# Optimization experiments

Measured on AMD Instinct MI355X. Metric: run time of the kernel, lower is better.

## Reference

```python
import jax, jax.numpy as jnp
import numpy as np

C = 512
NUM_GROUPS = 32
EPS = 1e-6


def setup_inputs() -> dict:
    key = jax.random.key(0)
    ks = jax.random.split(key, 10)
    x = jax.random.normal(ks[0], (2, C, 64, 64), dtype=jnp.float32)
    s = 1.0 / np.sqrt(C)
    return {
        "x": x,
        "gn_gamma": jnp.ones((C,), jnp.float32),
        "gn_beta": jnp.zeros((C,), jnp.float32),
        "wq": jax.random.normal(ks[1], (C, C), jnp.float32) * s,
        "bq": jnp.zeros((C,), jnp.float32),
        "wk": jax.random.normal(ks[2], (C, C), jnp.float32) * s,
        "bk": jnp.zeros((C,), jnp.float32),
        "wv": jax.random.normal(ks[3], (C, C), jnp.float32) * s,
        "bv": jnp.zeros((C,), jnp.float32),
        "wo": jax.random.normal(ks[4], (C, C), jnp.float32) * s,
        "bo": jnp.zeros((C,), jnp.float32),
    }


def group_norm(x, gamma, beta):
    b, c, h, w = x.shape
    xg = x.reshape(b, NUM_GROUPS, c // NUM_GROUPS, h, w)
    mean = xg.mean(axis=(2, 3, 4), keepdims=True)
    var = xg.var(axis=(2, 3, 4), keepdims=True)
    xg = (xg - mean) * jax.lax.rsqrt(var + EPS)
    x = xg.reshape(b, c, h, w)
    return x * gamma[None, :, None, None] + beta[None, :, None, None]


def conv1x1(x, w, bias):
    # 1x1 conv == channel matmul: (b,c,h,w),(o,c) -> (b,o,h,w)
    return jnp.einsum('bchw,oc->bohw', x, w) + bias[None, :, None, None]


def reference(x, gn_gamma, gn_beta, wq, bq, wk, bk, wv, bv, wo, bo):
    b, c, h, w = x.shape
    hn = group_norm(x, gn_gamma, gn_beta)
    q = conv1x1(hn, wq, bq).reshape(b, c, h * w)  # (b,c,n)
    k = conv1x1(hn, wk, bk).reshape(b, c, h * w)
    v = conv1x1(hn, wv, bv).reshape(b, c, h * w)
    scale = int(c) ** (-0.5)
    # scores[b,i,j] = sum_c q[b,c,i] k[b,c,j]
    scores = jnp.einsum('bci,bcj->bij', q, k) * scale
    attn = jax.nn.softmax(scores, axis=2)
    out = jnp.einsum('bcj,bij->bci', v, attn).reshape(b, c, h, w)
    out = conv1x1(out, wo, bo)
    return x + out
```

## Files before the change

### kernel.cpp

```cpp
#include <hip/hip_runtime.h>

typedef unsigned short ushort_t;
typedef unsigned char uchar_t;
typedef __bf16 bf16x8 __attribute__((ext_vector_type(8)));
typedef float f32x4 __attribute__((ext_vector_type(4)));

__device__ __forceinline__ ushort_t f2bf(float f) {
  unsigned u = __float_as_uint(f);
  u += 0x7fff + ((u >> 16) & 1);
  return (ushort_t)(u >> 16);
}

__device__ __forceinline__ void gload16(const void* g, void* l) {
  __builtin_amdgcn_global_load_lds(
      (const __attribute__((address_space(1))) unsigned int*)g,
      (__attribute__((address_space(3))) unsigned int*)l, 16, 0, 0);
}

__global__ __launch_bounds__(256) void cvt_weights(
    const float* __restrict__ wq, const float* __restrict__ wk,
    const float* __restrict__ wv, const float* __restrict__ wo,
    const float* __restrict__ bq, const float* __restrict__ bk,
    ushort_t* __restrict__ dst, float* __restrict__ qkbias,
    float* __restrict__ stats2) {
  int b = blockIdx.x, t = threadIdx.x;
  if (b < 1024) {
    int i = b * 256 + t;
    dst[i]          = f2bf(wq[i]);
    dst[262144 + i] = f2bf(wk[i]);
    dst[524288 + i] = f2bf(wv[i]);
    dst[786432 + i] = f2bf(wo[i]);
  } else if (b < 1028) {
    int j = (b - 1024) * 256 + t;
    qkbias[j] = (j < 512) ? bq[j] : bk[j - 512];
  } else {
    if (t < 128) stats2[t] = 0.f;
  }
}

__global__ __launch_bounds__(256) void zero_f32(float* __restrict__ p) {
  p[blockIdx.x * 256 + threadIdx.x] = 0.f;
}

__global__ __launch_bounds__(256) void gn_stats_partial(const float* __restrict__ x,
                                                        float* __restrict__ stats2) {
  int bg = blockIdx.x >> 2, q = blockIdx.x & 3;
  const float4* p = (const float4*)(x + (size_t)bg * 65536 + q * 16384);
  float s = 0.f, ss = 0.f;
  for (int i = threadIdx.x; i < 4096; i += 256) {
    float4 v = p[i];
    s += v.x + v.y + v.z + v.w;
    ss += v.x * v.x + v.y * v.y + v.z * v.z + v.w * v.w;
  }
  for (int off = 32; off; off >>= 1) {
    s += __shfl_xor(s, off, 64);
    ss += __shfl_xor(ss, off, 64);
  }
  __shared__ float sh[8];
  int wave = threadIdx.x >> 6, lane = threadIdx.x & 63;
  if (lane == 0) { sh[wave] = s; sh[4 + wave] = ss; }
  __syncthreads();
  if (threadIdx.x == 0) {
    atomicAdd(&stats2[bg * 2], sh[0] + sh[1] + sh[2] + sh[3]);
    atomicAdd(&stats2[bg * 2 + 1], sh[4] + sh[5] + sh[6] + sh[7]);
  }
}

__global__ __launch_bounds__(64) void gn_finalize(const float* __restrict__ stats2,
                                                  float* __restrict__ stats) {
  int t = threadIdx.x;
  float s = stats2[t * 2], ss = stats2[t * 2 + 1];
  float mean = s * (1.f / 65536.f);
  float var = ss * (1.f / 65536.f) - mean * mean;
  stats[t * 2] = mean;
  stats[t * 2 + 1] = rsqrtf(var + 1e-6f);
}

__global__ __launch_bounds__(256) void gn_apply(
    const float* __restrict__ x, const float* __restrict__ gamma,
    const float* __restrict__ beta, const float* __restrict__ stats,
    ushort_t* __restrict__ hnT) {
  __shared__ float T[32][33];
  int i0 = blockIdx.x * 32, c0 = blockIdx.y * 32, b = blockIdx.z;
  int tx = threadIdx.x, ty = threadIdx.y;
#pragma unroll
  for (int k = 0; k < 4; k++) {
    int cl = ty + k * 8;
    int c = c0 + cl;
    int bg = (b * 32 + (c >> 4)) * 2;
    float mean = stats[bg], rstd = stats[bg + 1];
    float v = x[((size_t)(b * 512 + c)) * 4096 + i0 + tx];
    T[cl][tx] = (v - mean) * rstd * gamma[c] + beta[c];
  }
  __syncthreads();
#pragma unroll
  for (int k = 0; k < 4; k++) {
    int il = ty + k * 8;
    hnT[((size_t)b * 4096 + i0 + il) * 512 + c0 + tx] = f2bf(T[tx][il]);
  }
}

template <int BN>
__global__ __launch_bounds__(256) void gemm_abt(
    const ushort_t* __restrict__ A, long long sA, int lda,
    const ushort_t* __restrict__ B, long long sB, int ldb,
    int K, int N, int ldc,
    ushort_t* __restrict__ outB, long long sC,
    const float* __restrict__ bias, int bias_mode, float scale,
    float* __restrict__ outF, const float* __restrict__ resid,
    float* __restrict__ rowsum, const float* __restrict__ colscale,
    int swiz, int omode) {
  constexpr int CPW = (8 + BN / 16) / 4;
  constexpr int SB = (128 + BN) * 32;
  constexpr int MI = (BN == 128) ? 4 : 2;
  constexpr int NI = 4;
  __shared__ __align__(16) ushort_t Ls[2][SB];

  int bx = blockIdx.x, by = blockIdx.y, bz = blockIdx.z;
  if (swiz) {
    unsigned nx = gridDim.x, ny = gridDim.y;
    unsigned id = (blockIdx.z * ny + blockIdx.y) * nx + blockIdx.x;
    unsigned pb8 = (nx * ny) >> 3;
    unsigned c = id & 7, j = id >> 3;
    bz = j / pb8;
    unsigned jb = j - bz * pb8;
    unsigned jy = jb / nx;
    by = c * (ny >> 3) + jy;
    bx = jb - jy * nx;
  }

  int m0 = by * 128, n0 = bx * BN;
  int t = threadIdx.x;
  int lane = t & 63;
  int quad = lane >> 4, l16 = lane & 15;
  int wave = t >> 6;
  int wm = (BN == 128) ? (wave >> 1) * 64 : wave * 32;
  int wn = (BN == 128) ? (wave & 1) * 64 : 0;

  f32x4 acc[MI][NI];
#pragma unroll
  for (int i = 0; i < MI; i++)
#pragma unroll
    for (int j = 0; j < NI; j++)
#pragma unroll
      for (int r = 0; r < 4; r++) acc[i][j][r] = 0.f;

  const ushort_t* gp[CPW];
  int lofs[CPW];
  int crow = lane >> 2, skoff = (lane & 3) * 8;
#pragma unroll
  for (int i = 0; i < CPW; i++) {
    int c = wave * CPW + i;
    if (c < 8) {
      gp[i] = A + (size_t)bz * sA + (size_t)(m0 + c * 16 + crow) * lda + skoff;
      lofs[i] = c * 1024 + lane * 16;
    } else {
      int slot = (c - 8) * 16 + crow;
      int arow = (slot & ~63) + ((slot & 15) * 4) + ((slot & 63) >> 4);
      gp[i] = B + (size_t)bz * sB + (size_t)(n0 + arow) * ldb + skoff;
      lofs[i] = 8192 + (c - 8) * 1024 + lane * 16;
    }
  }
  char* lbase = (char*)&Ls[0][0];

#pragma unroll
  for (int i = 0; i < CPW; i++) gload16(gp[i], lbase + lofs[i]);

  for (int k0 = 0; k0 < K; k0 += 32) {
    int p = (k0 >> 5) & 1;
    __syncthreads();
    if (k0 + 32 < K) {
      int pofs = (p ^ 1) * (SB * 2);
#pragma unroll
      for (int i = 0; i < CPW; i++) gload16(gp[i] + k0 + 32, lbase + pofs + lofs[i]);
    }
    bf16x8 af[MI], bfr[NI];
#pragma unroll
    for (int i = 0; i < MI; i++)
      af[i] = *(const bf16x8*)&Ls[p][(wm + i * 16 + l16) * 32 + quad * 8];
#pragma unroll
    for (int j = 0; j < NI; j++)
      bfr[j] = *(const bf16x8*)&Ls[p][4096 + (wn + j * 16 + l16) * 32 + quad * 8];
#pragma unroll
    for (int mi = 0; mi < MI; mi++)
#pragma unroll
      for (int ni = 0; ni < NI; ni++)
        acc[mi][ni] = __builtin_amdgcn_mfma_f32_16x16x32_bf16(af[mi], bfr[ni], acc[mi][ni], 0, 0, 0);
  }

  size_t cbase = (size_t)bz * sC;
  int gnb = n0 + wn + l16 * 4;
  float cs4[4] = {1.f, 1.f, 1.f, 1.f};
  if (colscale) {
    float4 c4 = *(const float4*)&colscale[(size_t)bz * N + gnb];
    cs4[0] = 1.f / c4.x; cs4[1] = 1.f / c4.y; cs4[2] = 1.f / c4.z; cs4[3] = 1.f / c4.w;
  }
  float b4[4] = {0.f, 0.f, 0.f, 0.f};
  if (bias_mode == 2) {
    float4 t4 = *(const float4*)&bias[gnb];
    b4[0] = t4.x; b4[1] = t4.y; b4[2] = t4.z; b4[3] = t4.w;
  }
#pragma unroll
  for (int mi = 0; mi < MI; mi++) {
#pragma unroll
    for (int r = 0; r < 4; r++) {
      int m = m0 + wm + mi * 16 + quad * 4 + r;
      float rbias = (bias_mode == 1) ? bias[m] : 0.f;
      float v4[4];
      float rs = 0.f;
#pragma unroll
      for (int ni = 0; ni < NI; ni++) {
        float val = acc[mi][ni][r];
        if (colscale) val *= cs4[ni];
        val += (bias_mode == 2) ? b4[ni] : rbias;
        val *= scale;
        if (rowsum) { val = __expf(val) * 0.0625f; rs += val; }
        v4[ni] = val;
      }
      size_t idx = cbase + (size_t)m * ldc + gnb;
      if (omode == 1) {
        float4 rv = *(const float4*)&resid[idx];
        float4 ov = make_float4(v4[0] + rv.x, v4[1] + rv.y, v4[2] + rv.z, v4[3] + rv.w);
        *(float4*)&outF[idx] = ov;
      } else if (omode == 2) {
        unsigned w = __builtin_amdgcn_cvt_pk_fp8_f32(v4[0], v4[1], 0u, false);
        w = __builtin_amdgcn_cvt_pk_fp8_f32(v4[2], v4[3], w, true);
        *(unsigned*)&((uchar_t*)outB)[idx] = w;
      } else {
        unsigned lo = (unsigned)f2bf(v4[0]) | ((unsigned)f2bf(v4[1]) << 16);
        unsigned hi = (unsigned)f2bf(v4[2]) | ((unsigned)f2bf(v4[3]) << 16);
        *(uint2*)&outB[idx] = make_uint2(lo, hi);
      }
      if (rowsum) {
        rs += __shfl_xor(rs, 1, 64);
        rs += __shfl_xor(rs, 2, 64);
        rs += __shfl_xor(rs, 4, 64);
        rs += __shfl_xor(rs, 8, 64);
        if (l16 == 0) atomicAdd(&rowsum[(size_t)bz * 4096 + m], rs);
      }
    }
  }
}

template <int BN>
__global__ __launch_bounds__(256) void gemm_fp8(
    const uchar_t* __restrict__ A, long long sA, int lda,
    const uchar_t* __restrict__ B, long long sB, int ldb,
    int K, int ldc,
    void* __restrict__ outp, long long sC,
    float scale, float* __restrict__ rowsum, int swiz, int omode) {
  constexpr int CPW = (8 + BN / 16) / 4;
  constexpr int SBB = (128 + BN) * 64;
  constexpr int MI = (BN == 128) ? 4 : 2;
  constexpr int NI = 4;
  __shared__ __align__(16) uchar_t Ls[2][SBB];

  int bx = blockIdx.x, by = blockIdx.y, bz = blockIdx.z;
  if (swiz) {
    unsigned nx = gridDim.x, ny = gridDim.y;
    unsigned id = (blockIdx.z * ny + blockIdx.y) * nx + blockIdx.x;
    unsigned pb8 = (nx * ny) >> 3;
    unsigned c = id & 7, j = id >> 3;
    bz = j / pb8;
    unsigned jb = j - bz * pb8;
    unsigned jy = jb / nx;
    by = c * (ny >> 3) + jy;
    bx = jb - jy * nx;
  }

  int m0 = by * 128, n0 = bx * BN;
  int t = threadIdx.x;
  int lane = t & 63;
  int quad = lane >> 4, l16 = lane & 15;
  int wave = t >> 6;
  int wm = (BN == 128) ? (wave >> 1) * 64 : wave * 32;
  int wn = (BN == 128) ? (wave & 1) * 64 : 0;

  f32x4 acc[MI][NI];
#pragma unroll
  for (int i = 0; i < MI; i++)
#pragma unroll
    for (int j = 0; j < NI; j++)
#pragma unroll
      for (int r = 0; r < 4; r++) acc[i][j][r] = 0.f;

  const uchar_t* gp[CPW];
  int lofs[CPW];
  int r16 = lane & 15, sseg = (lane >> 4) * 16;
#pragma unroll
  for (int i = 0; i < CPW; i++) {
    int c = wave * CPW + i;
    if (c < 8) {
      gp[i] = A + (size_t)bz * sA + (size_t)(m0 + c * 16 + r16) * lda + sseg;
      lofs[i] = c * 1024 + lane * 16;
    } else {
      int slot = (c - 8) * 16 + r16;
      int arow = (slot & ~63) + ((slot & 15) * 4) + ((slot & 63) >> 4);
      gp[i] = B + (size_t)bz * sB + (size_t)(n0 + arow) * ldb + sseg;
      lofs[i] = 8192 + (c - 8) * 1024 + lane * 16;
    }
  }
  char* lbase = (char*)&Ls[0][0];

#pragma unroll
  for (int i = 0; i < CPW; i++) gload16(gp[i], lbase + lofs[i]);

  int vbase = l16 * 16 + (quad >> 1) * 256 + (quad & 1) * 8;
  for (int k0 = 0; k0 < K; k0 += 64) {
    int p = (k0 >> 6) & 1;
    __syncthreads();
    if (k0 + 64 < K) {
      int pofs = (p ^ 1) * SBB;
#pragma unroll
      for (int i = 0; i < CPW; i++) gload16(gp[i] + k0 + 64, lbase + pofs + lofs[i]);
    }
    const uchar_t* Lp = &Ls[p][0];
    long long af[2][MI], bfv[2][NI];
#pragma unroll
    for (int s = 0; s < 2; s++) {
#pragma unroll
      for (int i = 0; i < MI; i++)
        af[s][i] = *(const long long*)&Lp[wm * 64 + i * 1024 + s * 512 + vbase];
#pragma unroll
      for (int j = 0; j < NI; j++)
        bfv[s][j] = *(const long long*)&Lp[8192 + wn * 64 + j * 1024 + s * 512 + vbase];
    }
#pragma unroll
    for (int s = 0; s < 2; s++)
#pragma unroll
      for (int mi = 0; mi < MI; mi++)
#pragma unroll
        for (int ni = 0; ni < NI; ni++)
          acc[mi][ni] = __builtin_amdgcn_mfma_f32_16x16x32_fp8_fp8(af[s][mi], bfv[s][ni], acc[mi][ni], 0, 0, 0);
  }

  size_t cbase = (size_t)bz * sC;
  int gnb = n0 + wn + l16 * 4;
#pragma unroll
  for (int mi = 0; mi < MI; mi++) {
#pragma unroll
    for (int r = 0; r < 4; r++) {
      int m = m0 + wm + mi * 16 + quad * 4 + r;
      if (omode == 2) {
        float v4[4];
        float rs = 0.f;
#pragma unroll
        for (int ni = 0; ni < NI; ni++) {
          v4[ni] = __expf(acc[mi][ni][r] * scale) * 0.0625f;
          rs += v4[ni];
        }
        unsigned w = __builtin_amdgcn_cvt_pk_fp8_f32(v4[0], v4[1], 0u, false);
        w = __builtin_amdgcn_cvt_pk_fp8_f32(v4[2], v4[3], w, true);
        *(unsigned*)&((uchar_t*)outp)[cbase + (size_t)m * ldc + gnb] = w;
        rs += __shfl_xor(rs, 1, 64);
        rs += __shfl_xor(rs, 2, 64);
        rs += __shfl_xor(rs, 4, 64);
        rs += __shfl_xor(rs, 8, 64);
        if (l16 == 0) atomicAdd(&rowsum[(size_t)bz * 4096 + m], rs);
      } else {
        unsigned lo = (unsigned)f2bf(acc[mi][0][r]) | ((unsigned)f2bf(acc[mi][1][r]) << 16);
        unsigned hi = (unsigned)f2bf(acc[mi][2][r]) | ((unsigned)f2bf(acc[mi][3][r]) << 16);
        *(uint2*)&((ushort_t*)outp)[cbase + (size_t)m * ldc + gnb] = make_uint2(lo, hi);
      }
    }
  }
}

extern "C" void kernel_launch(void* const* d_in, const int* in_sizes, int n_in,
                              void* d_out, int out_size, void* d_ws, size_t ws_size,
                              hipStream_t stream) {
  const float* x     = (const float*)d_in[0];
  const float* gamma = (const float*)d_in[1];
  const float* beta  = (const float*)d_in[2];
  const float* wq    = (const float*)d_in[3];
  const float* bq    = (const float*)d_in[4];
  const float* wk    = (const float*)d_in[5];
  const float* bk    = (const float*)d_in[6];
  const float* wv    = (const float*)d_in[7];
  const float* bv    = (const float*)d_in[8];
  const float* wo    = (const float*)d_in[9];
  const float* bo    = (const float*)d_in[10];
  float* out = (float*)d_out;

  ushort_t* wb  = (ushort_t*)d_ws;
  ushort_t* wvb = wb + 524288;
  ushort_t* wob = wb + 786432;
  ushort_t* hnT = wb + 1048576;
  uchar_t*  qk8 = (uchar_t*)(hnT + 4194304);
  uchar_t*  vC8 = qk8 + 8388608;
  ushort_t* OT  = (ushort_t*)(vC8 + 4194304);
  uchar_t*  S8  = (uchar_t*)(OT + 4194304);
  float* fbuf   = (float*)(S8 + 33554432);
  float* stats  = fbuf;
  float* stats2 = fbuf + 128;
  float* qkbias = fbuf + 256;
  float* l      = (float*)hnT;

  const long long HS = 2097152;
  const long long QS = 4194304;
  const long long SS = 16777216;
  const float scale = 0.044194173824159216f;

  cvt_weights<<<dim3(1029), dim3(256), 0, stream>>>(wq, wk, wv, wo, bq, bk, wb, qkbias, stats2);
  gn_stats_partial<<<dim3(256), dim3(256), 0, stream>>>(x, stats2);
  gn_finalize<<<dim3(1), dim3(64), 0, stream>>>(stats2, stats);
  gn_apply<<<dim3(128, 16, 2), dim3(32, 8), 0, stream>>>(x, gamma, beta, stats, hnT);
  gemm_abt<128><<<dim3(8, 32, 2), dim3(256), 0, stream>>>(
      hnT, HS, 512, wb, 0, 512, 512, 1024, 1024, (ushort_t*)qk8, QS, qkbias, 2, 1.f,
      nullptr, nullptr, nullptr, nullptr, 1, 2);
  gemm_abt<64><<<dim3(64, 4, 2), dim3(256), 0, stream>>>(
      wvb, 0, 512, hnT, HS, 512, 512, 4096, 4096, (ushort_t*)vC8, HS, bv, 1, 1.f,
      nullptr, nullptr, nullptr, nullptr, 0, 2);
  zero_f32<<<dim3(32), dim3(256), 0, stream>>>(l);
  gemm_fp8<128><<<dim3(32, 32, 2), dim3(256), 0, stream>>>(
      qk8, QS, 1024, qk8 + 512, QS, 1024, 512, 4096, S8, SS, scale, l, 1, 2);
  gemm_fp8<64><<<dim3(8, 32, 2), dim3(256), 0, stream>>>(
      S8, SS, 4096, vC8, HS, 4096, 4096, 512, OT, HS, 1.f, nullptr, 1, 0);
  gemm_abt<64><<<dim3(64, 4, 2), dim3(256), 0, stream>>>(
      wob, 0, 512, OT, HS, 512, 512, 4096, 4096, nullptr, HS, bo, 1, 1.f,
      out, x, nullptr, l, 0, 1);
}
```

Baseline: 240.7 us.

## Move QKV projections to FP8 GEMMs and fold zeroing into weight conversion

The group-norm output and the Q/K/V weights are now stored as FP8, and the QK and V projections run through the FP8 GEMM kernel, which gains bias support. The separate zero kernel is folded into the weight-conversion launch, and the score GEMM switches from a 128-wide to a 64-wide tile. This halves the bytes moved for the projection inputs and uses the faster FP8 matrix path, at the cost of lower precision in Q, K and V.

```diff
diff --git a/kernel.cpp b/kernel.cpp
--- a/kernel.cpp
+++ b/kernel.cpp
@@ -11,6 +11,11 @@
   return (ushort_t)(u >> 16);
 }
 
+__device__ __forceinline__ uchar_t f2fp8(float v) {
+  unsigned w = __builtin_amdgcn_cvt_pk_fp8_f32(v, v, 0u, false);
+  return (uchar_t)(w & 0xff);
+}
+
 __device__ __forceinline__ void gload16(const void* g, void* l) {
   __builtin_amdgcn_global_load_lds(
       (const __attribute__((address_space(1))) unsigned int*)g,
@@ -21,25 +26,24 @@
     const float* __restrict__ wq, const float* __restrict__ wk,
     const float* __restrict__ wv, const float* __restrict__ wo,
     const float* __restrict__ bq, const float* __restrict__ bk,
-    ushort_t* __restrict__ dst, float* __restrict__ qkbias,
-    float* __restrict__ stats2) {
+    uchar_t* __restrict__ wqk8, uchar_t* __restrict__ wv8,
+    ushort_t* __restrict__ wob, float* __restrict__ qkbias,
+    float* __restrict__ stats2, float* __restrict__ l) {
   int b = blockIdx.x, t = threadIdx.x;
   if (b < 1024) {
     int i = b * 256 + t;
-    dst[i]          = f2bf(wq[i]);
-    dst[262144 + i] = f2bf(wk[i]);
-    dst[524288 + i] = f2bf(wv[i]);
-    dst[786432 + i] = f2bf(wo[i]);
+    wqk8[i]          = f2fp8(wq[i]);
+    wqk8[262144 + i] = f2fp8(wk[i]);
+    wv8[i]           = f2fp8(wv[i]);
+    wob[i]           = f2bf(wo[i]);
   } else if (b < 1028) {
     int j = (b - 1024) * 256 + t;
     qkbias[j] = (j < 512) ? bq[j] : bk[j - 512];
+  } else if (b == 1028) {
+    if (t < 128) stats2[t] = 0.f;
   } else {
-    if (t < 128) stats2[t] = 0.f;
-  }
-}
-
-__global__ __launch_bounds__(256) void zero_f32(float* __restrict__ p) {
-  p[blockIdx.x * 256 + threadIdx.x] = 0.f;
+    l[(b - 1029) * 256 + t] = 0.f;
+  }
 }
 
 __global__ __launch_bounds__(256) void gn_stats_partial(const float* __restrict__ x,
@@ -79,7 +83,7 @@
 __global__ __launch_bounds__(256) void gn_apply(
     const float* __restrict__ x, const float* __restrict__ gamma,
     const float* __restrict__ beta, const float* __restrict__ stats,
-    ushort_t* __restrict__ hnT) {
+    uchar_t* __restrict__ hn8) {
   __shared__ float T[32][33];
   int i0 = blockIdx.x * 32, c0 = blockIdx.y * 32, b = blockIdx.z;
   int tx = threadIdx.x, ty = threadIdx.y;
@@ -93,11 +97,11 @@
     T[cl][tx] = (v - mean) * rstd * gamma[c] + beta[c];
   }
   __syncthreads();
-#pragma unroll
-  for (int k = 0; k < 4; k++) {
-    int il = ty + k * 8;
-    hnT[((size_t)b * 4096 + i0 + il) * 512 + c0 + tx] = f2bf(T[tx][il]);
-  }
+  int t = ty * 32 + tx;
+  int il = t >> 3, cu = (t & 7) * 4;
+  unsigned w = __builtin_amdgcn_cvt_pk_fp8_f32(T[cu][il], T[cu + 1][il], 0u, false);
+  w = __builtin_amdgcn_cvt_pk_fp8_f32(T[cu + 2][il], T[cu + 3][il], w, true);
+  *(unsigned*)&hn8[((size_t)b * 4096 + i0 + il) * 512 + c0 + cu] = w;
 }
 
 template <int BN>
@@ -207,14 +211,12 @@
       int m = m0 + wm + mi * 16 + quad * 4 + r;
       float rbias = (bias_mode == 1) ? bias[m] : 0.f;
       float v4[4];
-      float rs = 0.f;
 #pragma unroll
       for (int ni = 0; ni < NI; ni++) {
         float val = acc[mi][ni][r];
         if (colscale) val *= cs4[ni];
         val += (bias_mode == 2) ? b4[ni] : rbias;
         val *= scale;
-        if (rowsum) { val = __expf(val) * 0.0625f; rs += val; }
         v4[ni] = val;
       }
       size_t idx = cbase + (size_t)m * ldc + gnb;
@@ -222,21 +224,10 @@
         float4 rv = *(const float4*)&resid[idx];
         float4 ov = make_float4(v4[0] + rv.x, v4[1] + rv.y, v4[2] + rv.z, v4[3] + rv.w);
         *(float4*)&outF[idx] = ov;
-      } else if (omode == 2) {
-        unsigned w = __builtin_amdgcn_cvt_pk_fp8_f32(v4[0], v4[1], 0u, false);
-        w = __builtin_amdgcn_cvt_pk_fp8_f32(v4[2], v4[3], w, true);
-        *(unsigned*)&((uchar_t*)outB)[idx] = w;
       } else {
         unsigned lo = (unsigned)f2bf(v4[0]) | ((unsigned)f2bf(v4[1]) << 16);
         unsigned hi = (unsigned)f2bf(v4[2]) | ((unsigned)f2bf(v4[3]) << 16);
         *(uint2*)&outB[idx] = make_uint2(lo, hi);
-      }
-      if (rowsum) {
-        rs += __shfl_xor(rs, 1, 64);
-        rs += __shfl_xor(rs, 2, 64);
-        rs += __shfl_xor(rs, 4, 64);
-        rs += __shfl_xor(rs, 8, 64);
-        if (l16 == 0) atomicAdd(&rowsum[(size_t)bz * 4096 + m], rs);
       }
     }
   }
@@ -248,7 +239,8 @@
     const uchar_t* __restrict__ B, long long sB, int ldb,
     int K, int ldc,
     void* __restrict__ outp, long long sC,
-    float scale, float* __restrict__ rowsum, int swiz, int omode) {
+    const float* __restrict__ bias, int bias_mode, float scale,
+    float* __restrict__ rowsum, int swiz, int omode) {
   constexpr int CPW = (8 + BN / 16) / 4;
   constexpr int SBB = (128 + BN) * 64;
   constexpr int MI = (BN == 128) ? 4 : 2;
@@ -336,31 +328,42 @@
 
   size_t cbase = (size_t)bz * sC;
   int gnb = n0 + wn + l16 * 4;
+  float b4[4] = {0.f, 0.f, 0.f, 0.f};
+  if (bias_mode == 2) {
+    float4 t4 = *(const float4*)&bias[gnb];
+    b4[0] = t4.x; b4[1] = t4.y; b4[2] = t4.z; b4[3] = t4.w;
+  }
 #pragma unroll
   for (int mi = 0; mi < MI; mi++) {
 #pragma unroll
     for (int r = 0; r < 4; r++) {
       int m = m0 + wm + mi * 16 + quad * 4 + r;
-      if (omode == 2) {
-        float v4[4];
-        float rs = 0.f;
-#pragma unroll
-        for (int ni = 0; ni < NI; ni++) {
-          v4[ni] = __expf(acc[mi][ni][r] * scale) * 0.0625f;
-          rs += v4[ni];
-        }
+      float rbias = (bias_mode == 1) ? bias[m] : 0.f;
+      float v4[4];
+      float rs = 0.f;
+#pragma unroll
+      for (int ni = 0; ni < NI; ni++) {
+        float val = acc[mi][ni][r];
+        val += (bias_mode == 2) ? b4[ni] : rbias;
+        if (omode == 2) { val = __expf(val * scale) * 0.0625f; rs += val; }
+        v4[ni] = val;
+      }
+      size_t idx = cbase + (size_t)m * ldc + gnb;
+      if (omode == 0) {
+        unsigned lo = (unsigned)f2bf(v4[0]) | ((unsigned)f2bf(v4[1]) << 16);
+        unsigned hi = (unsigned)f2bf(v4[2]) | ((unsigned)f2bf(v4[3]) << 16);
+        *(uint2*)&((ushort_t*)outp)[idx] = make_uint2(lo, hi);
+      } else {
         unsigned w = __builtin_amdgcn_cvt_pk_fp8_f32(v4[0], v4[1], 0u, false);
         w = __builtin_amdgcn_cvt_pk_fp8_f32(v4[2], v4[3], w, true);
-        *(unsigned*)&((uchar_t*)outp)[cbase + (size_t)m * ldc + gnb] = w;
+        *(unsigned*)&((uchar_t*)outp)[idx] = w;
+      }
+      if (omode == 2) {
         rs += __shfl_xor(rs, 1, 64);
         rs += __shfl_xor(rs, 2, 64);
         rs += __shfl_xor(rs, 4, 64);
         rs += __shfl_xor(rs, 8, 64);
         if (l16 == 0) atomicAdd(&rowsum[(size_t)bz * 4096 + m], rs);
-      } else {
-        unsigned lo = (unsigned)f2bf(acc[mi][0][r]) | ((unsigned)f2bf(acc[mi][1][r]) << 16);
-        unsigned hi = (unsigned)f2bf(acc[mi][2][r]) | ((unsigned)f2bf(acc[mi][3][r]) << 16);
-        *(uint2*)&((ushort_t*)outp)[cbase + (size_t)m * ldc + gnb] = make_uint2(lo, hi);
       }
     }
   }
@@ -382,41 +385,44 @@
   const float* bo    = (const float*)d_in[10];
   float* out = (float*)d_out;
 
-  ushort_t* wb  = (ushort_t*)d_ws;
-  ushort_t* wvb = wb + 524288;
-  ushort_t* wob = wb + 786432;
-  ushort_t* hnT = wb + 1048576;
-  uchar_t*  qk8 = (uchar_t*)(hnT + 4194304);
-  uchar_t*  vC8 = qk8 + 8388608;
-  ushort_t* OT  = (ushort_t*)(vC8 + 4194304);
-  uchar_t*  S8  = (uchar_t*)(OT + 4194304);
-  float* fbuf   = (float*)(S8 + 33554432);
+  uchar_t* base = (uchar_t*)d_ws;
+  uchar_t* wqk8 = base;
+  uchar_t* wv8  = base + 524288;
+  ushort_t* wob = (ushort_t*)(base + 786432);
+  uchar_t* hn8  = base + 1310720;
+  uchar_t* qk8  = base + 5505024;
+  uchar_t* vC8  = base + 13893632;
+  ushort_t* OT  = (ushort_t*)(base + 18087936);
+  uchar_t* S8   = base + 26476544;
+  float* fbuf   = (float*)(base + 60030976);
   float* stats  = fbuf;
   float* stats2 = fbuf + 128;
   float* qkbias = fbuf + 256;
-  float* l      = (float*)hnT;
-
-  const long long HS = 2097152;
-  const long long QS = 4194304;
-  const long long SS = 16777216;
+  float* l      = fbuf + 1280;
+
+  const long long HS8 = 2097152;
+  const long long QS8 = 4194304;
+  const long long SS8 = 16777216;
   const float scale = 0.044194173824159216f;
 
-  cvt_weights<<<dim3(1029), dim3(256), 0, stream>>>(wq, wk, wv, wo, bq, bk, wb, qkbias, stats2);
+  cvt_weights<<<dim3(1061), dim3(256), 0, stream>>>(
+      wq, wk, wv, wo, bq, bk, wqk8, wv8, wob, qkbias, stats2, l);
   gn_stats_partial<<<dim3(256), dim3(256), 0, stream>>>(x, stats2);
   gn_finalize<<<dim3(1), dim3(64), 0, stream>>>(stats2, stats);
-  gn_apply<<<dim3(128, 16, 2), dim3(32, 8), 0, stream>>>(x, gamma, beta, stats, hnT);
-  gemm_abt<128><<<dim3(8, 32, 2), dim3(256), 0, stream>>>(
-      hnT, HS, 512, wb, 0, 512, 512, 1024, 1024, (ushort_t*)qk8, QS, qkbias, 2, 1.f,
-      nullptr, nullptr, nullptr, nullptr, 1, 2);
+  gn_apply<<<dim3(128, 16, 2), dim3(32, 8), 0, stream>>>(x, gamma, beta, stats, hn8);
+  gemm_fp8<64><<<dim3(16, 32, 2), dim3(256), 0, stream>>>(
+      hn8, HS8, 512, wqk8, 0, 512, 512, 1024, qk8, QS8,
+      qkbias, 2, 1.f, nullptr, 1, 3);
+  gemm_fp8<64><<<dim3(64, 4, 2), dim3(256), 0, stream>>>(
+      wv8, 0, 512, hn8, HS8, 512, 512, 4096, vC8, HS8,
+      bv, 1, 1.f, nullptr, 0, 3);
+  gemm_fp8<64><<<dim3(64, 32, 2), dim3(256), 0, stream>>>(
+      qk8, QS8, 1024, qk8 + 512, QS8, 1024, 512, 4096, S8, SS8,
+      nullptr, 0, scale, l, 1, 2);
+  gemm_fp8<64><<<dim3(8, 32, 2), dim3(256), 0, stream>>>(
+      S8, SS8, 4096, vC8, HS8, 4096, 4096, 512, OT, HS8,
+      nullptr, 0, 1.f, nullptr, 1, 0);
   gemm_abt<64><<<dim3(64, 4, 2), dim3(256), 0, stream>>>(
-      wvb, 0, 512, hnT, HS, 512, 512, 4096, 4096, (ushort_t*)vC8, HS, bv, 1, 1.f,
-      nullptr, nullptr, nullptr, nullptr, 0, 2);
-  zero_f32<<<dim3(32), dim3(256), 0, stream>>>(l);
-  gemm_fp8<128><<<dim3(32, 32, 2), dim3(256), 0, stream>>>(
-      qk8, QS, 1024, qk8 + 512, QS, 1024, 512, 4096, S8, SS, scale, l, 1, 2);
-  gemm_fp8<64><<<dim3(8, 32, 2), dim3(256), 0, stream>>>(
-      S8, SS, 4096, vC8, HS, 4096, 4096, 512, OT, HS, 1.f, nullptr, 1, 0);
-  gemm_abt<64><<<dim3(64, 4, 2), dim3(256), 0, stream>>>(
-      wob, 0, 512, OT, HS, 512, 512, 4096, 4096, nullptr, HS, bo, 1, 1.f,
+      wob, 0, 512, OT, HS8, 512, 512, 4096, 4096, nullptr, HS8, bo, 1, 1.f,
       out, x, nullptr, l, 0, 1);
 }
```

Measured after the change: 250.5 us. 1.04x slower.
